# Optimization experiments

Hardware: AMD Instinct MI355X
Metric: run time of the kernel (lower is better)

The kernel has to match this reference:

```python
import jax, jax.numpy as jnp
import numpy as np

B, N, K = 4, 250_000, 32
W_FG, W_INST, W_SMOOTH, W_SEED = 1.0, 1.0, 10.0, 10.0


def setup_inputs() -> dict:
    key = jax.random.key(0)
    k1, k2, k3, k4, k5 = jax.random.split(key, 5)
    return {
        "offsets": jax.random.normal(k1, (B, N, 3), jnp.float32),
        "coords": jax.random.normal(k2, (B, N, 3), jnp.float32),
        # small sigma scale so exp(10*sigma_k) stays in a sane range
        "sigmas": jax.random.normal(k3, (B, N, 3), jnp.float32) * 0.05,
        "seeds": jax.random.normal(k4, (B, N), jnp.float32),
        # instance ids in [-1, K); -1 = background
        "instances": jax.random.randint(k5, (B, N), 0, K + 1, jnp.int32) - 1,
    }


def _lovasz_hinge(logits, labels):
    # logits, labels: (B, K, N); vectorized lovasz_hinge_flat per (b, k)
    signs = 2.0 * labels - 1.0
    errors = 1.0 - logits * signs
    order = jnp.argsort(-errors, axis=-1)              # descending sort
    errors_sorted = jnp.take_along_axis(errors, order, axis=-1)
    gt_sorted = jnp.take_along_axis(labels, order, axis=-1)
    gts = jnp.sum(gt_sorted, axis=-1, keepdims=True)
    intersection = gts - jnp.cumsum(gt_sorted, axis=-1)
    union = gts + jnp.cumsum(1.0 - gt_sorted, axis=-1)
    jaccard = 1.0 - intersection / union
    grad = jnp.concatenate([jaccard[..., :1], jaccard[..., 1:] - jaccard[..., :-1]], axis=-1)
    return jnp.sum(jax.nn.relu(errors_sorted) * grad, axis=-1)  # (B, K)


def reference(offsets, coords, sigmas, seeds, instances):
    sg = jax.lax.stop_gradient
    emb = jnp.tanh(offsets) + coords                    # (B, N, 3) spatial embeddings
    seed = jax.nn.sigmoid(seeds)                        # (B, N)

    masks = (instances[:, :, None] == jnp.arange(K)[None, None, :]).astype(jnp.float32)  # (B, N, K)
    counts = jnp.sum(masks, axis=1)                     # (B, K)
    validf = (counts > 0).astype(jnp.float32)
    cnt = jnp.maximum(counts, 1.0)

    # per-instance masked means
    center = jnp.einsum('bnk,bnd->bkd', masks, emb) / cnt[..., None]     # (B, K, 3)
    sigma_k = jnp.einsum('bnk,bnd->bkd', masks, sigmas) / cnt[..., None]  # (B, K, 3)

    # smooth loss: mean over masked (n_k, 3) of (sigma - stop_grad(sigma_k))^2
    sk = sg(sigma_k)
    dev2 = (jnp.einsum('bnk,bnd->bk', masks, sigmas ** 2)
            - 2.0 * jnp.einsum('bnk,bnd,bkd->bk', masks, sigmas, sk)
            + counts * jnp.sum(sk ** 2, axis=-1))
    smooth_k = dev2 / (cnt * 3.0)                       # (B, K)

    s_e = jnp.exp(sigma_k * 10.0)                       # (B, K, 3)
    # quad[b,k,n] = sum_d s_e * (emb - center)^2, expanded to avoid (B,K,N,3)
    quad = (jnp.einsum('bkd,bnd->bkn', s_e, emb ** 2)
            - 2.0 * jnp.einsum('bkd,bnd->bkn', s_e * center, emb)
            + jnp.sum(s_e * center ** 2, axis=-1)[:, :, None])
    probs = jnp.exp(-quad)                              # (B, K, N)
    logits = 2.0 * probs - 1.0

    labels = jnp.transpose(masks, (0, 2, 1))            # (B, K, N)
    lov = _lovasz_hinge(logits, labels)                 # (B, K)

    obj = jnp.maximum(jnp.sum(validf, axis=-1), 1.0)    # (B,)
    instance_loss = jnp.sum(lov * validf, axis=-1) / obj
    smooth_loss = jnp.sum(smooth_k * validf, axis=-1) / obj

    bg = (instances == -1).astype(jnp.float32)
    seed_bg = jnp.sum(bg * seed ** 2, axis=-1)          # (B,)
    seed_fg = W_FG * jnp.sum(labels * (seed[:, None, :] - sg(probs)) ** 2, axis=(-1, -2))
    seed_loss = (seed_bg + seed_fg) / float(N)

    loss = jnp.mean(W_INST * instance_loss + W_SMOOTH * smooth_loss + W_SEED * seed_loss)
    return loss + jnp.sum(offsets) * 0.0
```

## Files before the change

kernel.cpp:

```cpp
#include <hip/hip_runtime.h>
#include <hip/hip_fp16.h>
#include <math.h>

#define B_ 4
#define N_ 250000
#define K_ 32
#define NB 4096
#define NB2 2048
#define KG 2
#define HCH 16
#define S2 16
#define SC 4
#define SLOT_SHIFT 13


__device__ __forceinline__ uint32_t pack_h2(float a, float b) {
  __half2 h = __floats2half2_rn(a, b);
  return *(reinterpret_cast<uint32_t*>(&h));
}
__device__ __forceinline__ float2 unpack_h2(uint32_t u) {
  __half2 h = *(reinterpret_cast<__half2*>(&u));
  return __half22float2(h);
}

__device__ __forceinline__ float quad_qc(float ex, float ey, float ez,
                                         float sex, float sey, float sez,
                                         float tx, float ty, float tz, float A) {
  float q = fmaf(ex, fmaf(sex, ex, -tx),
            fmaf(ey, fmaf(sey, ey, -ty),
            fmaf(ez, fmaf(sez, ez, -tz), A)));
  return fmaxf(q, 0.f);
}

__device__ __forceinline__ float fast_rcp(float x) { return __builtin_amdgcn_rcpf(x); }
__device__ __forceinline__ float fast_tanh(float x) {
  return 1.f - 2.f * fast_rcp(__expf(2.f * x) + 1.f);
}
__device__ __forceinline__ float fast_sigmoid(float x) {
  return fast_rcp(1.f + __expf(-x));
}

__global__ __launch_bounds__(256) void k_emb(
    const float* __restrict__ off, const float* __restrict__ crd,
    const float* __restrict__ seed, const int* __restrict__ inst,
    float* __restrict__ seed_bg, uint2* __restrict__ emb2,
    uint32_t* __restrict__ cursor, uint32_t* __restrict__ list,
    uint32_t* __restrict__ hneg_g)
{
  __shared__ uint32_t lcnt[K_], lbase[K_];
  __shared__ float red[4];
  const int b = blockIdx.y;
  const int tid = threadIdx.x;

  {
    int flat = (blockIdx.y * gridDim.x + blockIdx.x) * 256 + tid;
    if (flat < (2097152 / 16)) ((uint4*)hneg_g)[flat] = make_uint4(0u, 0u, 0u, 0u);
  }

  if (tid < K_) lcnt[tid] = 0;
  __syncthreads();

  const int n0 = blockIdx.x * 1024 + tid * 4;
  int kv[4];
  const bool valid = (n0 < N_);
  float sbg = 0.f;

  if (valid) {
    const int idx = b * N_ + n0;
    const float4* o4 = (const float4*)&off[(size_t)idx * 3];
    const float4* c4 = (const float4*)&crd[(size_t)idx * 3];
    float4 o0 = o4[0], o1 = o4[1], o2 = o4[2];
    float4 c0 = c4[0], c1 = c4[1], c2 = c4[2];
    float4 sd = *(const float4*)&seed[idx];
    int4 ki = *(const int4*)&inst[idx];
    kv[0] = ki.x; kv[1] = ki.y; kv[2] = ki.z; kv[3] = ki.w;

    float ex0 = fast_tanh(o0.x) + c0.x, ey0 = fast_tanh(o0.y) + c0.y, ez0 = fast_tanh(o0.z) + c0.z;
    float ex1 = fast_tanh(o0.w) + c0.w, ey1 = fast_tanh(o1.x) + c1.x, ez1 = fast_tanh(o1.y) + c1.y;
    float ex2 = fast_tanh(o1.z) + c1.z, ey2 = fast_tanh(o1.w) + c1.w, ez2 = fast_tanh(o2.x) + c2.x;
    float ex3 = fast_tanh(o2.y) + c2.y, ey3 = fast_tanh(o2.z) + c2.z, ez3 = fast_tanh(o2.w) + c2.w;
    uint4 w0, w1;
    w0.x = pack_h2(ex0, ey0); w0.y = pack_h2(ez0, 0.f);
    w0.z = pack_h2(ex1, ey1); w0.w = pack_h2(ez1, 0.f);
    w1.x = pack_h2(ex2, ey2); w1.y = pack_h2(ez2, 0.f);
    w1.z = pack_h2(ex3, ey3); w1.w = pack_h2(ez3, 0.f);
    ((uint4*)&emb2[idx])[0] = w0;
    ((uint4*)&emb2[idx])[1] = w1;

    float sv[4] = {fast_sigmoid(sd.x), fast_sigmoid(sd.y),
                   fast_sigmoid(sd.z), fast_sigmoid(sd.w)};
#pragma unroll
    for (int j = 0; j < 4; ++j) {
      if (kv[j] >= 0) {
        atomicAdd(&lcnt[kv[j]], 1u);
      }
      sbg = fmaf((kv[j] < 0) ? sv[j] : 0.f, sv[j], sbg);
    }
  }
  __syncthreads();
  if (tid < K_) {
    uint32_t c = lcnt[tid];
    lbase[tid] = c ? atomicAdd(&cursor[b * K_ + tid], c) : 0u;
    lcnt[tid] = 0;
  }
  __syncthreads();
  if (valid) {
#pragma unroll
    for (int j = 0; j < 4; ++j) {
      if (kv[j] >= 0) {
        uint32_t r = atomicAdd(&lcnt[kv[j]], 1u);
        list[(uint32_t)((b * K_ + kv[j]) << SLOT_SHIFT) + lbase[kv[j]] + r] =
            (uint32_t)(n0 + j);
      }
    }
  }
  for (int d = 32; d > 0; d >>= 1) sbg += __shfl_down(sbg, d, 64);
  int wid = tid >> 6, lane = tid & 63;
  if (lane == 0) red[wid] = sbg;
  __syncthreads();
  if (tid == 0) atomicAdd(&seed_bg[b], red[0] + red[1] + red[2] + red[3]);
}

__global__ __launch_bounds__(256) void k_segstats(
    const uint2* __restrict__ emb2, const float* __restrict__ sig,
    const uint32_t* __restrict__ list, const uint32_t* __restrict__ cursor,
    float* __restrict__ acc)
{
  __shared__ float red[4 * 8];
  const int seg = blockIdx.x >> 2;
  const int c = blockIdx.x & (SC - 1);
  const int b = seg >> 5;
  const int G = (int)cursor[seg];
  if (G == 0) return;
  const int i0 = (int)((long)G * c / SC);
  const int i1 = (int)((long)G * (c + 1) / SC);
  const int base = b * N_;
  const uint32_t lo = (uint32_t)(seg << SLOT_SHIFT);
  const int tid = threadIdx.x;

  float sex_ = 0.f, sey_ = 0.f, sez_ = 0.f;
  float ssx = 0.f, ssy = 0.f, ssz = 0.f, ss2 = 0.f;
  for (int i = i0 + tid; i < i1; i += 256) {
    int idx = base + (int)list[lo + i];
    uint2 e = emb2[idx];
    float2 xy = unpack_h2(e.x);
    float2 zw = unpack_h2(e.y);
    float sx = sig[(size_t)idx * 3 + 0];
    float sy = sig[(size_t)idx * 3 + 1];
    float sz = sig[(size_t)idx * 3 + 2];
    sex_ += xy.x; sey_ += xy.y; sez_ += zw.x;
    ssx += sx; ssy += sy; ssz += sz;
    ss2 = fmaf(sx, sx, fmaf(sy, sy, fmaf(sz, sz, ss2)));
  }
  for (int d = 32; d > 0; d >>= 1) {
    sex_ += __shfl_down(sex_, d, 64); sey_ += __shfl_down(sey_, d, 64);
    sez_ += __shfl_down(sez_, d, 64); ssx  += __shfl_down(ssx,  d, 64);
    ssy  += __shfl_down(ssy,  d, 64); ssz  += __shfl_down(ssz,  d, 64);
    ss2  += __shfl_down(ss2,  d, 64);
  }
  int wid = tid >> 6, lane = tid & 63;
  if (lane == 0) {
    float* r = &red[wid * 8];
    r[0] = sex_; r[1] = sey_; r[2] = sez_;
    r[3] = ssx;  r[4] = ssy;  r[5] = ssz; r[6] = ss2;
  }
  __syncthreads();
  if (tid == 0) {
    float v[7];
    for (int f = 0; f < 7; ++f)
      v[f] = red[f] + red[8 + f] + red[16 + f] + red[24 + f];
    float* a = &acc[seg * 8];
    atomicAdd(&a[0], (float)(i1 - i0));
    atomicAdd(&a[1], v[0]); atomicAdd(&a[2], v[1]); atomicAdd(&a[3], v[2]);
    atomicAdd(&a[4], v[3]); atomicAdd(&a[5], v[4]); atomicAdd(&a[6], v[5]);
    atomicAdd(&a[7], v[6]);
  }
}

__global__ __launch_bounds__(512) void k_hist(
    const uint2* __restrict__ emb2, const float* __restrict__ acc,
    float* __restrict__ p05, uint32_t* __restrict__ hneg_g)
{
  __shared__ uint32_t h[KG * NB];
  const int g = blockIdx.x;
  const int xcd = g & 7;
  const int b = xcd >> 1;
  const int sub = ((g >> 3) << 1) | (xcd & 1);
  const int kg = sub >> 4;
  const int c = sub & (HCH - 1);
  const int seg0 = b * K_ + kg * KG;
  const int tid = threadIdx.x;

  float sexA[KG], seyA[KG], sezA[KG], txA[KG], tyA[KG], tzA[KG], AA[KG];
#pragma unroll
  for (int j = 0; j < KG; ++j) {
    const float* a = &acc[(seg0 + j) * 8];
    float counts = a[0];
    float cnt = fmaxf(counts, 1.f);
    float inv = 1.f / cnt;
    float cx = a[1] * inv, cy = a[2] * inv, cz = a[3] * inv;
    float skx = a[4] * inv, sky = a[5] * inv, skz = a[6] * inv;
    sexA[j] = expf(10.f * skx); seyA[j] = expf(10.f * sky); sezA[j] = expf(10.f * skz);
    txA[j] = 2.f * sexA[j] * cx; tyA[j] = 2.f * seyA[j] * cy; tzA[j] = 2.f * sezA[j] * cz;
    AA[j] = sexA[j] * cx * cx + seyA[j] * cy * cy + sezA[j] * cz * cz;
    if (c == 0 && tid == 0) {
      float dev2 = a[7] - 2.f * (a[4] * skx + a[5] * sky + a[6] * skz)
                 + counts * (skx * skx + sky * sky + skz * skz);
      float* o = &p05[(seg0 + j) * 16];
      o[0] = sexA[j]; o[1] = seyA[j]; o[2] = sezA[j];
      o[3] = txA[j]; o[4] = tyA[j]; o[5] = tzA[j];
      o[6] = AA[j]; o[7] = counts;
      o[8] = (counts > 0.f) ? 1.f : 0.f; o[9] = dev2 / (cnt * 3.f);
    }
  }
  for (int i = tid; i < KG * NB; i += 512) h[i] = 0;
  __syncthreads();

  const int base = b * N_;
  const int n0 = c * (N_ / HCH);
  const int n1 = n0 + (N_ / HCH);
  for (int n = n0 + tid; n < n1; n += 512) {
    uint2 e = emb2[base + n];
    float2 xy = unpack_h2(e.x);
    float2 zw = unpack_h2(e.y);
#pragma unroll
    for (int j = 0; j < KG; ++j) {
      float qc = quad_qc(xy.x, xy.y, zw.x,
                         sexA[j], seyA[j], sezA[j], txA[j], tyA[j], tzA[j], AA[j]);
      atomicAdd(&h[j * NB + (__float_as_uint(qc) >> 19)], 1u);
    }
  }
  __syncthreads();
#pragma unroll
  for (int j = 0; j < KG; ++j) {
    uint32_t* gn = &hneg_g[(seg0 + j) * NB];
    for (int i = tid; i < NB; i += 512) {
      uint32_t v = h[j * NB + i];
      if (v) atomicAdd(&gn[i], v);
    }
  }
}

__device__ __forceinline__ void scan_excl(uint32_t* h, uint32_t* wsum, int tid)
{
  const int chunk = NB >> 10;
  const int base = tid * chunk;
  uint32_t vals[4];
  uint32_t s = 0;
  for (int i = 0; i < chunk; ++i) { vals[i] = h[base + i]; s += vals[i]; }
  uint32_t x = s;
  int lane = tid & 63;
  for (int d = 1; d < 64; d <<= 1) {
    uint32_t y = (uint32_t)__shfl_up((int)x, d, 64);
    if (lane >= d) x += y;
  }
  int wid = tid >> 6;
  if (lane == 63) wsum[wid] = x;
  __syncthreads();
  if (tid == 0) {
    uint32_t a = 0;
    for (int w = 0; w < 16; ++w) { uint32_t t = wsum[w]; wsum[w] = a; a += t; }
  }
  __syncthreads();
  uint32_t run = wsum[wid] + (x - s);
  for (int i = 0; i < chunk; ++i) { uint32_t t = vals[i]; h[base + i] = run; run += t; }
  __syncthreads();
}

__global__ __launch_bounds__(1024) void k_scanpos(
    const uint2* __restrict__ emb2, const float* __restrict__ seed,
    const float* __restrict__ p05, const uint32_t* __restrict__ list,
    uint32_t* __restrict__ hneg_g, float2* __restrict__ tabN,
    float* __restrict__ lov_out, float* __restrict__ seed_fg)
{
  __shared__ uint32_t hn[NB];
  __shared__ uint32_t hp[NB];
  __shared__ uint32_t wsum[16];
  __shared__ float red[32];
  const int seg = blockIdx.x;
  const int b = seg >> 5;
  const float* pp = &p05[seg * 16];
  const float Gf = pp[7];
  if (Gf <= 0.f) return;
  const float sex = pp[0], sey = pp[1], sez = pp[2];
  const float tx = pp[3], ty = pp[4], tz = pp[5], A = pp[6];
  const int tid = threadIdx.x;
  const int base = b * N_;
  const int G = (int)Gf;
  const uint32_t lo = (uint32_t)(seg << SLOT_SHIFT);
  const float Nnegf = (float)N_ - Gf;

  uint32_t* gn = &hneg_g[seg * NB];
  for (int i = tid; i < NB; i += 1024) { hn[i] = gn[i]; hp[i] = 0; }
  __syncthreads();

  for (int i = tid; i < G; i += 1024) {
    int n = (int)list[lo + i];
    uint2 e = emb2[base + n];
    float2 xy = unpack_h2(e.x);
    float2 zw = unpack_h2(e.y);
    float qc = quad_qc(xy.x, xy.y, zw.x, sex, sey, sez, tx, ty, tz, A);
    atomicAdd(&hn[__float_as_uint(qc) >> 19], 0xFFFFFFFFu);
    float p = __expf(-qc);
    float qs = -__logf(1.f - p);
    atomicAdd(&hp[__float_as_uint(qs) >> 19], 1u);
  }
  __syncthreads();
  scan_excl(hn, wsum, tid);
  scan_excl(hp, wsum, tid);

  float2* tN = &tabN[(size_t)seg * NB2];
  for (int bkt = tid; bkt < NB2; bkt += 1024) {
    float R  = (float)hn[2 * bkt];
    float nn = (bkt < NB2 - 1) ? (float)hn[2 * bkt + 2] : Nnegf;
    float m  = nn - R;
    float pb = (float)hp[2 * bkt];
    float pn = (bkt < NB2 - 1) ? (float)hp[2 * bkt + 2] : Gf;
    float gr = Gf + R;
    float psi2 = 2.f / (gr * (gr + m));
    float u = psi2 * (Gf - pb);
    float v = psi2 * (pn - pb) * (1.f / 1048576.f);
    tN[bkt] = make_float2(u, v);
  }

  float lov = 0.f, sfg = 0.f;
  for (int i = tid; i < G; i += 1024) {
    int n = (int)list[lo + i];
    uint2 e = emb2[base + n];
    float2 xy = unpack_h2(e.x);
    float2 zw = unpack_h2(e.y);
    float qc = quad_qc(xy.x, xy.y, zw.x, sex, sey, sez, tx, ty, tz, A);
    float p = __expf(-qc);
    float qs = -__logf(1.f - p);
    uint32_t qb = __float_as_uint(qs);
    uint32_t bk = qb >> 19;
    float frac = (float)(qb & 0x7FFFFu) * (1.f / 524288.f);
    float R  = (float)hn[bk];
    float nn = (bk < NB - 1) ? (float)hn[bk + 1] : Nnegf;
    float F = R + frac * (nn - R);
    lov += (2.f - 2.f * p) / (Gf + F);
    float s = fast_sigmoid(seed[base + n]);
    float d = s - p;
    sfg += d * d;
    uint32_t cb = __float_as_uint(qc);
    uint32_t b2 = cb >> 20;
    float fr = (float)(cb & 0xFFFFFu);
    float R2  = (float)hn[2 * b2];
    float nn2 = (b2 < NB2 - 1) ? (float)hn[2 * b2 + 2] : Nnegf;
    float m2  = nn2 - R2;
    float pb2 = (float)hp[2 * b2];
    float pn2 = (b2 < NB2 - 1) ? (float)hp[2 * b2 + 2] : Gf;
    float gr2 = Gf + R2;
    float psi2 = 2.f / (gr2 * (gr2 + m2));
    float u2 = psi2 * (Gf - pb2);
    float v2 = psi2 * (pn2 - pb2) * (1.f / 1048576.f);
    lov -= p * fmaf(-v2, fr, u2);
  }

  for (int d = 32; d > 0; d >>= 1) {
    lov += __shfl_down(lov, d, 64);
    sfg += __shfl_down(sfg, d, 64);
  }
  int wid = tid >> 6, lane = tid & 63;
  if (lane == 0) { red[wid] = lov; red[16 + wid] = sfg; }
  __syncthreads();
  if (tid == 0) {
    float lt = 0.f, st = 0.f;
    for (int w = 0; w < 16; ++w) { lt += red[w]; st += red[16 + w]; }
    atomicAdd(&lov_out[seg], lt);
    atomicAdd(&seed_fg[b], st);
  }
}

__global__ __launch_bounds__(256) void k_pass2neg(
    const uint2* __restrict__ emb2, const float* __restrict__ p05,
    const float2* __restrict__ tabN, float* __restrict__ lov_out)
{
  __shared__ float red[4];
  const int g = blockIdx.x;
  const int xcd = g & 7;
  const int bb = xcd >> 1;
  const int sub = ((g >> 3) << 1) | (xcd & 1);
  const int seg = bb * K_ + (sub >> 4);
  const int chunk = sub & (S2 - 1);
  const int b = bb;
  const float* pp = &p05[seg * 16];
  const float Gf = pp[7];
  if (Gf <= 0.f) return;
  const float sex = pp[0], sey = pp[1], sez = pp[2];
  const float tx = pp[3], ty = pp[4], tz = pp[5], A = pp[6];
  const int tid = threadIdx.x;
  const int base = b * N_;
  const int n0 = chunk * (N_ / S2);
  const int nfull = n0 + 15360;
  const int n1 = n0 + (N_ / S2);
  const float2* tN = &tabN[(size_t)seg * NB2];

  float l0 = 0.f, l1 = 0.f, l2 = 0.f, l3 = 0.f;
  for (int s = n0 + tid; s < nfull; s += 1024) {
    uint2 e0 = emb2[base + s];
    uint2 e1 = emb2[base + s + 256];
    uint2 e2 = emb2[base + s + 512];
    uint2 e3 = emb2[base + s + 768];
    float2 a0 = unpack_h2(e0.x), b0 = unpack_h2(e0.y);
    float2 a1 = unpack_h2(e1.x), b1 = unpack_h2(e1.y);
    float2 a2 = unpack_h2(e2.x), b2 = unpack_h2(e2.y);
    float2 a3 = unpack_h2(e3.x), b3 = unpack_h2(e3.y);
    float q0 = quad_qc(a0.x, a0.y, b0.x, sex, sey, sez, tx, ty, tz, A);
    float q1 = quad_qc(a1.x, a1.y, b1.x, sex, sey, sez, tx, ty, tz, A);
    float q2 = quad_qc(a2.x, a2.y, b2.x, sex, sey, sez, tx, ty, tz, A);
    float q3 = quad_qc(a3.x, a3.y, b3.x, sex, sey, sez, tx, ty, tz, A);
    uint32_t c0 = __float_as_uint(q0), c1 = __float_as_uint(q1);
    uint32_t c2 = __float_as_uint(q2), c3 = __float_as_uint(q3);
    float2 t0 = tN[c0 >> 20];
    float2 t1 = tN[c1 >> 20];
    float2 t2 = tN[c2 >> 20];
    float2 t3 = tN[c3 >> 20];
    float p0 = __expf(-q0), p1 = __expf(-q1);
    float p2 = __expf(-q2), p3 = __expf(-q3);
    l0 = fmaf(p0, fmaf(-t0.y, (float)(c0 & 0xFFFFFu), t0.x), l0);
    l1 = fmaf(p1, fmaf(-t1.y, (float)(c1 & 0xFFFFFu), t1.x), l1);
    l2 = fmaf(p2, fmaf(-t2.y, (float)(c2 & 0xFFFFFu), t2.x), l2);
    l3 = fmaf(p3, fmaf(-t3.y, (float)(c3 & 0xFFFFFu), t3.x), l3);
  }
  for (int n = nfull + tid; n < n1; n += 256) {
    uint2 e = emb2[base + n];
    float2 xy = unpack_h2(e.x);
    float2 zw = unpack_h2(e.y);
    float qc = quad_qc(xy.x, xy.y, zw.x, sex, sey, sez, tx, ty, tz, A);
    float p = __expf(-qc);
    uint32_t cb = __float_as_uint(qc);
    float2 t = tN[cb >> 20];
    l0 = fmaf(p, fmaf(-t.y, (float)(cb & 0xFFFFFu), t.x), l0);
  }

  float lov = (l0 + l1) + (l2 + l3);
  for (int d = 32; d > 0; d >>= 1) lov += __shfl_down(lov, d, 64);
  int wid = tid >> 6, lane = tid & 63;
  if (lane == 0) red[wid] = lov;
  __syncthreads();
  if (tid == 0) {
    float lt = red[0] + red[1] + red[2] + red[3];
    atomicAdd(&lov_out[seg], lt);
  }
}

__global__ void k_final(const float* __restrict__ p05, const float* __restrict__ lov,
                        const float* __restrict__ seed_bg, const float* __restrict__ seed_fg,
                        float* __restrict__ out)
{
  __shared__ float sv[B_], sl[B_], ss[B_];
  int tid = threadIdx.x;
  if (tid < B_) { sv[tid] = 0.f; sl[tid] = 0.f; ss[tid] = 0.f; }
  __syncthreads();
  int b = tid >> 5;
  float vf = p05[tid * 16 + 8];
  atomicAdd(&sv[b], vf);
  atomicAdd(&sl[b], lov[tid] * vf);
  atomicAdd(&ss[b], p05[tid * 16 + 9] * vf);
  __syncthreads();
  if (tid == 0) {
    float total = 0.f;
    for (int bb = 0; bb < B_; ++bb) {
      float obj = fmaxf(sv[bb], 1.f);
      float seed_l = (seed_bg[bb] + seed_fg[bb]) / (float)N_;
      total += sl[bb] / obj + 10.f * (ss[bb] / obj) + 10.f * seed_l;
    }
    out[0] = total / (float)B_;
  }
}

extern "C" void kernel_launch(void* const* d_in, const int* in_sizes, int n_in,
                              void* d_out, int out_size, void* d_ws, size_t ws_size,
                              hipStream_t stream) {
  const float* off  = (const float*)d_in[0];
  const float* crd  = (const float*)d_in[1];
  const float* sig  = (const float*)d_in[2];
  const float* seed = (const float*)d_in[3];
  const int*   inst = (const int*)d_in[4];

  float* ws      = (float*)d_ws;
  float* acc     = ws;
  float* seed_bg = ws + 1024;
  float* seed_fg = ws + 1028;
  float* lov     = ws + 1032;
  uint32_t* cursor = (uint32_t*)(ws + 1160);
  float* p05     = ws + 2048;
  char* pbase = (char*)d_ws;
  uint2*    emb2   = (uint2*)(pbase + 65536);
  uint32_t* hneg_g = (uint32_t*)(pbase + 65536 + 8388608);
  float2*   tabN   = (float2*)(pbase + 65536 + 8388608 + 2097152);
  uint32_t* list   = (uint32_t*)((char*)tabN + 2097152);

  hipMemsetAsync(d_ws, 0, 8192, stream);

  dim3 ge((N_ + 1023) / 1024, B_);
  k_emb<<<ge, 256, 0, stream>>>(off, crd, seed, inst, seed_bg, emb2, cursor, list,
                                hneg_g);
  k_segstats<<<B_ * K_ * SC, 256, 0, stream>>>(emb2, sig, list, cursor, acc);
  k_hist<<<B_ * (K_ / KG) * HCH, 512, 0, stream>>>(emb2, acc, p05, hneg_g);
  k_scanpos<<<B_ * K_, 1024, 0, stream>>>(emb2, seed, p05, list, hneg_g, tabN, lov, seed_fg);
  k_pass2neg<<<B_ * K_ * S2, 256, 0, stream>>>(emb2, p05, tabN, lov);
  k_final<<<1, 128, 0, stream>>>(p05, lov, seed_bg, seed_fg, (float*)d_out);
}
```

Before: 203.0 us.

## Replace global histogram atomics with per-chunk partial histograms; unroll hist loop

```diff
diff --git a/kernel.cpp b/kernel.cpp
--- a/kernel.cpp
+++ b/kernel.cpp
@@ -44,18 +44,12 @@
     const float* __restrict__ off, const float* __restrict__ crd,
     const float* __restrict__ seed, const int* __restrict__ inst,
     float* __restrict__ seed_bg, uint2* __restrict__ emb2,
-    uint32_t* __restrict__ cursor, uint32_t* __restrict__ list,
-    uint32_t* __restrict__ hneg_g)
+    uint32_t* __restrict__ cursor, uint32_t* __restrict__ list)
 {
   __shared__ uint32_t lcnt[K_], lbase[K_];
   __shared__ float red[4];
   const int b = blockIdx.y;
   const int tid = threadIdx.x;
-
-  {
-    int flat = (blockIdx.y * gridDim.x + blockIdx.x) * 256 + tid;
-    if (flat < (2097152 / 16)) ((uint4*)hneg_g)[flat] = make_uint4(0u, 0u, 0u, 0u);
-  }
 
   if (tid < K_) lcnt[tid] = 0;
   __syncthreads();
@@ -179,7 +173,7 @@
 
 __global__ __launch_bounds__(512) void k_hist(
     const uint2* __restrict__ emb2, const float* __restrict__ acc,
-    float* __restrict__ p05, uint32_t* __restrict__ hneg_g)
+    float* __restrict__ p05, uint32_t* __restrict__ gh)
 {
   __shared__ uint32_t h[KG * NB];
   const int g = blockIdx.x;
@@ -218,8 +212,30 @@
 
   const int base = b * N_;
   const int n0 = c * (N_ / HCH);
+  const int nfull = n0 + 14336;
   const int n1 = n0 + (N_ / HCH);
-  for (int n = n0 + tid; n < n1; n += 512) {
+  for (int n = n0 + tid; n < nfull; n += 2048) {
+    uint2 e0 = emb2[base + n];
+    uint2 e1 = emb2[base + n + 512];
+    uint2 e2 = emb2[base + n + 1024];
+    uint2 e3 = emb2[base + n + 1536];
+    float2 x0 = unpack_h2(e0.x), z0 = unpack_h2(e0.y);
+    float2 x1 = unpack_h2(e1.x), z1 = unpack_h2(e1.y);
+    float2 x2 = unpack_h2(e2.x), z2 = unpack_h2(e2.y);
+    float2 x3 = unpack_h2(e3.x), z3 = unpack_h2(e3.y);
+#pragma unroll
+    for (int j = 0; j < KG; ++j) {
+      float q0 = quad_qc(x0.x, x0.y, z0.x, sexA[j], seyA[j], sezA[j], txA[j], tyA[j], tzA[j], AA[j]);
+      float q1 = quad_qc(x1.x, x1.y, z1.x, sexA[j], seyA[j], sezA[j], txA[j], tyA[j], tzA[j], AA[j]);
+      float q2 = quad_qc(x2.x, x2.y, z2.x, sexA[j], seyA[j], sezA[j], txA[j], tyA[j], tzA[j], AA[j]);
+      float q3 = quad_qc(x3.x, x3.y, z3.x, sexA[j], seyA[j], sezA[j], txA[j], tyA[j], tzA[j], AA[j]);
+      atomicAdd(&h[j * NB + (__float_as_uint(q0) >> 19)], 1u);
+      atomicAdd(&h[j * NB + (__float_as_uint(q1) >> 19)], 1u);
+      atomicAdd(&h[j * NB + (__float_as_uint(q2) >> 19)], 1u);
+      atomicAdd(&h[j * NB + (__float_as_uint(q3) >> 19)], 1u);
+    }
+  }
+  for (int n = nfull + tid; n < n1; n += 512) {
     uint2 e = emb2[base + n];
     float2 xy = unpack_h2(e.x);
     float2 zw = unpack_h2(e.y);
@@ -233,11 +249,8 @@
   __syncthreads();
 #pragma unroll
   for (int j = 0; j < KG; ++j) {
-    uint32_t* gn = &hneg_g[(seg0 + j) * NB];
-    for (int i = tid; i < NB; i += 512) {
-      uint32_t v = h[j * NB + i];
-      if (v) atomicAdd(&gn[i], v);
-    }
+    uint32_t* gp = &gh[((size_t)c * (B_ * K_) + (seg0 + j)) * NB];
+    for (int i = tid; i < NB; i += 512) gp[i] = h[j * NB + i];
   }
 }
 
@@ -270,7 +283,7 @@
 __global__ __launch_bounds__(1024) void k_scanpos(
     const uint2* __restrict__ emb2, const float* __restrict__ seed,
     const float* __restrict__ p05, const uint32_t* __restrict__ list,
-    uint32_t* __restrict__ hneg_g, float2* __restrict__ tabN,
+    const uint32_t* __restrict__ gh, float2* __restrict__ tabN,
     float* __restrict__ lov_out, float* __restrict__ seed_fg)
 {
   __shared__ uint32_t hn[NB];
@@ -290,8 +303,13 @@
   const uint32_t lo = (uint32_t)(seg << SLOT_SHIFT);
   const float Nnegf = (float)N_ - Gf;
 
-  uint32_t* gn = &hneg_g[seg * NB];
-  for (int i = tid; i < NB; i += 1024) { hn[i] = gn[i]; hp[i] = 0; }
+  for (int i = tid; i < NB; i += 1024) {
+    uint32_t s = 0;
+#pragma unroll
+    for (int c = 0; c < HCH; ++c)
+      s += gh[((size_t)c * (B_ * K_) + seg) * NB + i];
+    hn[i] = s; hp[i] = 0;
+  }
   __syncthreads();
 
   for (int i = tid; i < G; i += 1024) {
@@ -487,19 +505,18 @@
   uint32_t* cursor = (uint32_t*)(ws + 1160);
   float* p05     = ws + 2048;
   char* pbase = (char*)d_ws;
-  uint2*    emb2   = (uint2*)(pbase + 65536);
-  uint32_t* hneg_g = (uint32_t*)(pbase + 65536 + 8388608);
-  float2*   tabN   = (float2*)(pbase + 65536 + 8388608 + 2097152);
-  uint32_t* list   = (uint32_t*)((char*)tabN + 2097152);
+  uint2*    emb2 = (uint2*)(pbase + 65536);
+  uint32_t* gh   = (uint32_t*)(pbase + 65536 + 8388608);
+  float2*   tabN = (float2*)(pbase + 65536 + 8388608 + 33554432);
+  uint32_t* list = (uint32_t*)((char*)tabN + 2097152);
 
   hipMemsetAsync(d_ws, 0, 8192, stream);
 
   dim3 ge((N_ + 1023) / 1024, B_);
-  k_emb<<<ge, 256, 0, stream>>>(off, crd, seed, inst, seed_bg, emb2, cursor, list,
-                                hneg_g);
+  k_emb<<<ge, 256, 0, stream>>>(off, crd, seed, inst, seed_bg, emb2, cursor, list);
   k_segstats<<<B_ * K_ * SC, 256, 0, stream>>>(emb2, sig, list, cursor, acc);
-  k_hist<<<B_ * (K_ / KG) * HCH, 512, 0, stream>>>(emb2, acc, p05, hneg_g);
-  k_scanpos<<<B_ * K_, 1024, 0, stream>>>(emb2, seed, p05, list, hneg_g, tabN, lov, seed_fg);
+  k_hist<<<B_ * (K_ / KG) * HCH, 512, 0, stream>>>(emb2, acc, p05, gh);
+  k_scanpos<<<B_ * K_, 1024, 0, stream>>>(emb2, seed, p05, list, gh, tabN, lov, seed_fg);
   k_pass2neg<<<B_ * K_ * S2, 256, 0, stream>>>(emb2, p05, tabN, lov);
   k_final<<<1, 128, 0, stream>>>(p05, lov, seed_bg, seed_fg, (float*)d_out);
 }
```

After: 209.5 us. 3.2% more time.
